# Kernel tuning notes

Hardware: AMD Instinct MI355X
Metric: run time of the kernel (lower is better)

## Reference

```python
import jax, jax.numpy as jnp
import numpy as np

B, S, D = 1, 2048, 4096
HQ, HK, HD = 32, 8, 128


def setup_inputs() -> dict:
    key = jax.random.key(0)
    ks = jax.random.split(key, 6)
    x = jax.random.normal(ks[0], (B, S, D), jnp.float32) * 0.02
    wq = jax.random.normal(ks[1], (D, HQ * HD), jnp.float32) * 0.02
    wk = jax.random.normal(ks[2], (D, HK * HD), jnp.float32) * 0.02
    wv = jax.random.normal(ks[3], (D, HK * HD), jnp.float32) * 0.02
    wo = jax.random.normal(ks[4], (HQ * HD, D), jnp.float32) * 0.02
    # canonical RoPE frequencies: theta = 10000
    inv_freq = 1.0 / (10000.0 ** (jnp.arange(0, HD, 2, dtype=jnp.float32) / HD))  # [HD/2]
    t = jnp.arange(S, dtype=jnp.float32)
    ang = jnp.outer(t, inv_freq)  # [S, HD/2]
    return {
        "x": x,
        "freqs_cos": jnp.cos(ang),
        "freqs_sin": jnp.sin(ang),
        "wq": wq, "wk": wk, "wv": wv, "wo": wo,
    }


def _rope(t, cos, sin):
    # t: [B, S, H, HD]; pairs are consecutive elements (view_as_complex semantics)
    tr = t.reshape(*t.shape[:-1], HD // 2, 2)
    t0, t1 = tr[..., 0], tr[..., 1]
    c = cos[None, :, None, :]
    s = sin[None, :, None, :]
    o0 = t0 * c - t1 * s
    o1 = t0 * s + t1 * c
    return jnp.stack([o0, o1], axis=-1).reshape(t.shape)


def reference(x, freqs_cos, freqs_sin, wq, wk, wv, wo):
    b, s, _ = x.shape
    g = HQ // HK  # GQA group size
    xq = (x @ wq).reshape(b, s, HQ, HD)
    xk = (x @ wk).reshape(b, s, HK, HD)
    xv = (x @ wv).reshape(b, s, HK, HD)
    xq = _rope(xq, freqs_cos, freqs_sin)
    xk = _rope(xk, freqs_cos, freqs_sin)
    scale = 1.0 / jnp.sqrt(jnp.float32(HD))
    xqg = xq.reshape(b, s, HK, g, HD)
    # scores: [b, HK, g, s_q, s_k]
    scores = jnp.einsum("bqkgd,bnkd->bkgqn", xqg, xk) * scale
    causal = jnp.tril(jnp.ones((s, s), dtype=bool))
    scores = jnp.where(causal[None, None, None, :, :], scores, -jnp.inf)
    p = jax.nn.softmax(scores, axis=-1)
    out = jnp.einsum("bkgqn,bnkd->bqkgd", p, xv).reshape(b, s, HQ * HD)
    return out @ wo
```

## Files before the change

kernel.cpp:

```cpp
#include <hip/hip_runtime.h>
#include <stdint.h>

typedef __bf16 bf16_t;
typedef bf16_t bf16x8 __attribute__((ext_vector_type(8)));
typedef float f32x4 __attribute__((ext_vector_type(4)));
typedef unsigned int u32;
typedef unsigned short u16;

#define DEV_INLINE __device__ __forceinline__

#define S_LEN 2048
#define D_MODEL 4096
#define HQ 32
#define HK 8
#define HD 128
#define NQKV 6144

DEV_INLINE u16 f2bf(float x) {
  union { float f; uint32_t u; } v; v.f = x;
  uint32_t r = v.u + 0x7FFFu + ((v.u >> 16) & 1u);
  return (u16)(r >> 16);
}
DEV_INLINE float bf2f(u16 x) {
  union { uint32_t u; float f; } v; v.u = ((uint32_t)x) << 16;
  return v.f;
}
DEV_INLINE u32 pack2bf(float a, float b) {
  return (u32)f2bf(a) | ((u32)f2bf(b) << 16);
}

DEV_INLINE void async_load16(const void* g, void* l) {
  __builtin_amdgcn_global_load_lds(
      (const __attribute__((address_space(1))) u32*)g,
      (__attribute__((address_space(3))) u32*)l, 16, 0, 0);
}

DEV_INLINE f32x4 mfma16(bf16x8 a, bf16x8 b, f32x4 c) {
  return __builtin_amdgcn_mfma_f32_16x16x32_bf16(a, b, c, 0, 0, 0);
}

__global__ void cvt_f32_bf16(const float* __restrict__ in, u16* __restrict__ out, int n) {
  int i = (blockIdx.x * blockDim.x + threadIdx.x) * 4;
  if (i >= n) return;
  float4 v = *(const float4*)(in + i);
  union { u16 s[4]; uint2 u; } o;
  o.s[0] = f2bf(v.x); o.s[1] = f2bf(v.y); o.s[2] = f2bf(v.z); o.s[3] = f2bf(v.w);
  *(uint2*)(out + i) = o.u;
}

__global__ void transpose_f32_bf16(const float* __restrict__ in, u16* __restrict__ out,
                                   int R, int C) {
  __shared__ float tile[32][33];
  int tx = threadIdx.x, ty = threadIdx.y;
  int c0 = blockIdx.x * 32, r0 = blockIdx.y * 32;
#pragma unroll
  for (int i = 0; i < 4; ++i)
    tile[ty + i * 8][tx] = in[(long)(r0 + ty + i * 8) * C + c0 + tx];
  __syncthreads();
#pragma unroll
  for (int i = 0; i < 4; ++i)
    out[(long)(c0 + ty + i * 8) * R + r0 + tx] = f2bf(tile[tx][ty + i * 8]);
}

__global__ void transpose_bf16(const u16* __restrict__ in, u16* __restrict__ out,
                               int R, int C, int ld_in, int col_off) {
  __shared__ u16 tile[32][33];
  int tx = threadIdx.x, ty = threadIdx.y;
  int c0 = blockIdx.x * 32, r0 = blockIdx.y * 32;
#pragma unroll
  for (int i = 0; i < 4; ++i)
    tile[ty + i * 8][tx] = in[(long)(r0 + ty + i * 8) * ld_in + col_off + c0 + tx];
  __syncthreads();
#pragma unroll
  for (int i = 0; i < 4; ++i)
    out[(long)(c0 + ty + i * 8) * R + r0 + tx] = tile[tx][ty + i * 8];
}

__global__ void rope_bf16(const u16* __restrict__ in, const float* __restrict__ cosb,
                          const float* __restrict__ sinb, u16* __restrict__ out,
                          int H, int ld_in, int col_off, float scale) {
  int idx = blockIdx.x * blockDim.x + threadIdx.x;
  int j = idx & 63;
  int sh = idx >> 6;
  int s = sh / H, h = sh - s * H;
  const u16* ip = in + (long)s * ld_in + col_off + h * HD;
  union { u32 u; u16 s2[2]; } v; v.u = *(const u32*)(ip + 2 * j);
  float q0 = bf2f(v.s2[0]), q1 = bf2f(v.s2[1]);
  float c = cosb[s * 64 + j], sn = sinb[s * 64 + j];
  union { u16 s2[2]; u32 u; } o;
  o.s2[0] = f2bf((q0 * c - q1 * sn) * scale);
  o.s2[1] = f2bf((q0 * sn + q1 * c) * scale);
  *(u32*)(out + (long)sh * HD + 2 * j) = o.u;
}

#define BARRIER() asm volatile("s_barrier" ::: "memory")
#define WAIT_LGKM0()                                            \
  do {                                                          \
    asm volatile("s_waitcnt lgkmcnt(0)" ::: "memory");          \
    __builtin_amdgcn_sched_barrier(0);                          \
  } while (0)
#define WAIT_VM(N) asm volatile("s_waitcnt vmcnt(" #N ")" ::: "memory")

#define PHASE_A(T, DO_STAGE)                                                      \
  {                                                                               \
    const u16* Ab_ = &lds[(T) & 3][0];                                            \
    const u16* Bb_ = &lds[(T) & 3][8192];                                         \
    bf16x8 af_[MFH];                                                              \
    _Pragma("unroll")                                                             \
    for (int i = 0; i < MFH; ++i) af_[i] = rdfrag(Ab_, wr * MROWS + i * 16 + l15);\
    _Pragma("unroll")                                                             \
    for (int j = 0; j < 4; ++j) bfr[j] = rdfrag(Bb_, wc * 64 + j * 16 + l15);     \
    if (DO_STAGE) stageA((T) + 3);                                                \
    BARRIER();                                                                    \
    WAIT_LGKM0();                                                                 \
    __builtin_amdgcn_s_setprio(1);                                                \
    _Pragma("unroll")                                                             \
    for (int i = 0; i < MFH; ++i)                                                 \
      _Pragma("unroll")                                                           \
      for (int j = 0; j < 4; ++j) acc[i][j] = mfma16(af_[i], bfr[j], acc[i][j]);  \
    __builtin_amdgcn_s_setprio(0);                                                \
    BARRIER();                                                                    \
  }

#define PHASE_B(T, DO_STAGE, VMWAIT)                                              \
  {                                                                               \
    const u16* Ab_ = &lds[(T) & 3][0];                                            \
    bf16x8 af_[MFH];                                                              \
    _Pragma("unroll")                                                             \
    for (int i = 0; i < MFH; ++i)                                                 \
      af_[i] = rdfrag(Ab_, wr * MROWS + (MFH + i) * 16 + l15);                    \
    if (DO_STAGE) stageB((T) + 3);                                                \
    BARRIER();                                                                    \
    WAIT_LGKM0();                                                                 \
    __builtin_amdgcn_s_setprio(1);                                                \
    _Pragma("unroll")                                                             \
    for (int i = 0; i < MFH; ++i)                                                 \
      _Pragma("unroll")                                                           \
      for (int j = 0; j < 4; ++j)                                                 \
        acc[MFH + i][j] = mfma16(af_[i], bfr[j], acc[MFH + i][j]);                \
    __builtin_amdgcn_s_setprio(0);                                                \
    VMWAIT;                                                                       \
    BARRIER();                                                                    \
  }

template <int BN, int WM, bool BF16OUT>
__global__ __launch_bounds__(512, 2) void gemm_pipe(
    const u16* __restrict__ A, const u16* __restrict__ Bt, void* __restrict__ Cv,
    int N, int K) {
  constexpr int WN = 8 / WM;
  constexpr int MROWS = 256 / WM;
  constexpr int MF = MROWS / 16;
  constexpr int MFH = MF / 2;
  constexpr int BPT = (BN * 4) / 512;
  constexpr int LDSU = (256 + BN) * 32;

  __shared__ __attribute__((aligned(16))) u16 lds[4][LDSU];

  const int tid = threadIdx.x;
  const int lane = tid & 63;
  const int wave = tid >> 6;
  const int quad = lane >> 4, l15 = lane & 15;
  const int wr = wave / WN, wc = wave % WN;

  const int gx = gridDim.x;
  const int bid = blockIdx.y * gx + blockIdx.x;
  const int cpx = (gx * gridDim.y) >> 3;
  const int sw = (bid & 7) * cpx + (bid >> 3);
  const int bn = sw % gx, bm = sw / gx;

  const long arow = (long)bm * 256, brow = (long)bn * BN;
  const int NT = K >> 5;

  auto stageA = [&](int ts) {
    const int bs = ts & 3;
    const int k0 = ts * 32;
#pragma unroll
    for (int j = 0; j < 2; ++j) {
      int c = tid + j * 512;
      int row = c >> 2, cc = c & 3, cs = cc ^ ((row >> 1) & 3);
      async_load16(A + (arow + row) * (long)K + k0 + cs * 8,
                   (u16*)&lds[bs][0] + c * 8);
    }
  };
  auto stageB = [&](int ts) {
    const int bs = ts & 3;
    const int k0 = ts * 32;
#pragma unroll
    for (int j = 0; j < BPT; ++j) {
      int c = tid + j * 512;
      int row = c >> 2, cc = c & 3, cs = cc ^ ((row >> 1) & 3);
      async_load16(Bt + (brow + row) * (long)K + k0 + cs * 8,
                   (u16*)&lds[bs][8192] + c * 8);
    }
  };
  auto rdfrag = [&](const u16* base, int row) -> bf16x8 {
    return *(const bf16x8*)(base + row * 32 + ((quad ^ ((row >> 1) & 3)) * 8));
  };

  f32x4 acc[MF][4] = {};
  bf16x8 bfr[4];

  stageA(0); stageB(0); stageA(1); stageB(1); stageA(2); stageB(2);
  if constexpr (BN == 256) { WAIT_VM(8); } else { WAIT_VM(6); }
  BARRIER();

  int t = 0;
  for (; t < NT - 3; ++t) {
    PHASE_A(t, true);
    if constexpr (BN == 256) { PHASE_B(t, true, WAIT_VM(8)); }
    else                     { PHASE_B(t, true, WAIT_VM(6)); }
  }
  PHASE_A(t, false);
  if constexpr (BN == 256) { PHASE_B(t, false, WAIT_VM(4)); }
  else                     { PHASE_B(t, false, WAIT_VM(3)); }
  ++t;
  PHASE_A(t, false);
  PHASE_B(t, false, WAIT_VM(0));
  ++t;
  PHASE_A(t, false);
  PHASE_B(t, false, ((void)0));

#pragma unroll
  for (int i = 0; i < MF; ++i) {
    const long row = (long)bm * 256 + wr * MROWS + i * 16 + quad * 4;
#pragma unroll
    for (int j = 0; j < 4; ++j) {
      const int col = bn * BN + wc * 64 + j * 16 + l15;
      if constexpr (BF16OUT) {
        u16* C = (u16*)Cv;
#pragma unroll
        for (int r = 0; r < 4; ++r) C[(row + r) * N + col] = f2bf(acc[i][j][r]);
      } else {
        float* C = (float*)Cv;
#pragma unroll
        for (int r = 0; r < 4; ++r) C[(row + r) * N + col] = acc[i][j][r];
      }
    }
  }
}

#define NEG_INF -1e30f
__global__ __launch_bounds__(256, 2) void attn_fwd(
    const u16* __restrict__ Qb, const u16* __restrict__ Kb,
    const u16* __restrict__ Vt, u16* __restrict__ Ob) {
  __shared__ __attribute__((aligned(16))) u16 Ks[2][64 * 128];
  __shared__ __attribute__((aligned(16))) u16 Vs[2][128 * 64];
  __shared__ __attribute__((aligned(16))) u16 Pts[4][16 * 64];
  const int tid = threadIdx.x;
  const int lane = tid & 63, wave = tid >> 6;
  const int quad = lane >> 4, l15 = lane & 15;
  const int lin = blockIdx.y * gridDim.x + blockIdx.x;
  const int h = lin & 31;
  const int pp = (lin >> 5) & 7;
  const int u = (lin >> 8) ? 15 - pp : pp;
  const int hk = h >> 2;
  const int swz = 2 * (l15 & 7);
  const int nt = 2 * (u + 1);

  bf16x8 qf[2][4];
#pragma unroll
  for (int n = 0; n < 2; ++n) {
    const u16* qrow = Qb + (long)(u * 128 + wave * 32 + n * 16 + l15) * (HQ * HD)
                      + h * HD + quad * 8;
#pragma unroll
    for (int ks = 0; ks < 4; ++ks) qf[n][ks] = *(const bf16x8*)(qrow + ks * 32);
  }

  auto stage = [&](int t) {
    const int b = t & 1;
#pragma unroll
    for (int it = 0; it < 4; ++it) {
      int c = tid + it * 256;
      int row = c >> 4, cc = c & 15, cs = cc ^ (row & 15);
      async_load16(Kb + (long)(t * 64 + row) * (HK * HD) + hk * HD + cs * 8,
                   (u16*)&Ks[b][0] + c * 8);
    }
#pragma unroll
    for (int it = 0; it < 4; ++it) {
      int c = tid + it * 256;
      int row = c >> 3, cc = c & 7, cs = cc ^ (row & 7);
      async_load16(Vt + (long)(hk * HD + row) * S_LEN + t * 64 + cs * 8,
                   (u16*)&Vs[b][0] + c * 8);
    }
  };

  float m_run[2] = {NEG_INF, NEG_INF}, l_run[2] = {0.f, 0.f};
  f32x4 oacc[8][2] = {};

  stage(0);
  __syncthreads();

  for (int t = 0; t < nt; ++t) {
    const int cur = t & 1;
    if (t + 1 < nt) stage(t + 1);

    if (t * 64 <= u * 128 + wave * 32 + 31) {
      f32x4 sc[4][2] = {};
      __builtin_amdgcn_s_setprio(1);
#pragma unroll
      for (int ks = 0; ks < 4; ++ks)
#pragma unroll
        for (int tj = 0; tj < 4; ++tj) {
          int row = tj * 16 + l15;
          bf16x8 kf = *(const bf16x8*)(&Ks[cur][0] + row * 128
                                       + (((ks * 4 + quad) ^ (row & 15)) * 8));
          sc[tj][0] = mfma16(kf, qf[0][ks], sc[tj][0]);
          sc[tj][1] = mfma16(kf, qf[1][ks], sc[tj][1]);
        }
      __builtin_amdgcn_s_setprio(0);

      const bool diag = (t >= 2 * u);
      const int kbase = t * 64 - u * 128;
#pragma unroll
      for (int n = 0; n < 2; ++n) {
        int qloc = wave * 32 + n * 16 + l15;
        if (diag) {
#pragma unroll
          for (int tj = 0; tj < 4; ++tj)
#pragma unroll
            for (int r = 0; r < 4; ++r)
              if (kbase + tj * 16 + quad * 4 + r > qloc) sc[tj][n][r] = NEG_INF;
        }
        float m = NEG_INF;
#pragma unroll
        for (int tj = 0; tj < 4; ++tj)
#pragma unroll
          for (int r = 0; r < 4; ++r) m = fmaxf(m, sc[tj][n][r]);
        m = fmaxf(m, __shfl_xor(m, 16));
        m = fmaxf(m, __shfl_xor(m, 32));
        if (!__all(m - m_run[n] <= 8.0f)) {
          float mnew = fmaxf(m_run[n], m);
          float alpha = __expf(m_run[n] - mnew);
          m_run[n] = mnew;
          l_run[n] *= alpha;
#pragma unroll
          for (int tj = 0; tj < 8; ++tj) oacc[tj][n] *= alpha;
        }
        float rs = 0.f;
#pragma unroll
        for (int tj = 0; tj < 4; ++tj)
#pragma unroll
          for (int r = 0; r < 4; ++r) {
            float p = __expf(sc[tj][n][r] - m_run[n]);
            sc[tj][n][r] = p;
            rs += p;
          }
        rs += __shfl_xor(rs, 16);
        rs += __shfl_xor(rs, 32);
        l_run[n] += rs;
      }

      u16* pw = &Pts[wave][0];
      bf16x8 pf0[2], pf1[2];
#pragma unroll
      for (int tj = 0; tj < 4; ++tj) {
        union { u32 w[2]; uint2 u2; } pk;
        pk.w[0] = pack2bf(sc[tj][0][0], sc[tj][0][1]);
        pk.w[1] = pack2bf(sc[tj][0][2], sc[tj][0][3]);
        *(uint2*)(pw + l15 * 64 + (((tj * 4 + quad) ^ swz) * 4)) = pk.u2;
      }
      __asm__ volatile("s_waitcnt lgkmcnt(0)" ::: "memory");
#pragma unroll
      for (int ks = 0; ks < 2; ++ks)
        pf0[ks] = *(const bf16x8*)(pw + l15 * 64 + (((ks * 8 + quad * 2) ^ swz) * 4));
      __asm__ volatile("s_waitcnt lgkmcnt(0)" ::: "memory");
#pragma unroll
      for (int tj = 0; tj < 4; ++tj) {
        union { u32 w[2]; uint2 u2; } pk;
        pk.w[0] = pack2bf(sc[tj][1][0], sc[tj][1][1]);
        pk.w[1] = pack2bf(sc[tj][1][2], sc[tj][1][3]);
        *(uint2*)(pw + l15 * 64 + (((tj * 4 + quad) ^ swz) * 4)) = pk.u2;
      }
      __asm__ volatile("s_waitcnt lgkmcnt(0)" ::: "memory");
#pragma unroll
      for (int ks = 0; ks < 2; ++ks)
        pf1[ks] = *(const bf16x8*)(pw + l15 * 64 + (((ks * 8 + quad * 2) ^ swz) * 4));

      __builtin_amdgcn_s_setprio(1);
#pragma unroll
      for (int ks = 0; ks < 2; ++ks)
#pragma unroll
        for (int tj = 0; tj < 8; ++tj) {
          int row = tj * 16 + l15;
          bf16x8 vf = *(const bf16x8*)(&Vs[cur][0] + row * 64
                                       + (((ks * 4 + quad) ^ (row & 7)) * 8));
          oacc[tj][0] = mfma16(vf, pf0[ks], oacc[tj][0]);
          oacc[tj][1] = mfma16(vf, pf1[ks], oacc[tj][1]);
        }
      __builtin_amdgcn_s_setprio(0);
    }

    __syncthreads();
  }

#pragma unroll
  for (int n = 0; n < 2; ++n) {
    float inv_l = 1.0f / l_run[n];
    long grow = u * 128 + wave * 32 + n * 16 + l15;
#pragma unroll
    for (int tj = 0; tj < 8; ++tj) {
      int gcol = h * HD + tj * 16 + quad * 4;
      union { u32 w[2]; uint2 u2; } pk;
      pk.w[0] = pack2bf(oacc[tj][n][0] * inv_l, oacc[tj][n][1] * inv_l);
      pk.w[1] = pack2bf(oacc[tj][n][2] * inv_l, oacc[tj][n][3] * inv_l);
      *(uint2*)(Ob + grow * (HQ * HD) + gcol) = pk.u2;
    }
  }
}

#define MB (1024L * 1024L)

extern "C" void kernel_launch(void* const* d_in, const int* in_sizes, int n_in,
                              void* d_out, int out_size, void* d_ws, size_t ws_size,
                              hipStream_t stream) {
  const float* x    = (const float*)d_in[0];
  const float* fcos = (const float*)d_in[1];
  const float* fsin = (const float*)d_in[2];
  const float* wq   = (const float*)d_in[3];
  const float* wk   = (const float*)d_in[4];
  const float* wv   = (const float*)d_in[5];
  const float* wo   = (const float*)d_in[6];
  float* out = (float*)d_out;

  char* ws = (char*)d_ws;
  u16* wt    = (u16*)(ws + 0 * MB);
  u16* xb    = (u16*)(ws + 48 * MB);
  u16* QKVb  = (u16*)(ws + 64 * MB);
  u16* Qb    = (u16*)(ws + 88 * MB);
  u16* Kb    = (u16*)(ws + 104 * MB);
  u16* Vt    = (u16*)(ws + 108 * MB);
  u16* attnb = (u16*)(ws + 112 * MB);

  const int M = S_LEN, D = D_MODEL;

  cvt_f32_bf16<<<(M * D) / 1024, 256, 0, stream>>>(x, xb, M * D);

  transpose_f32_bf16<<<dim3(D / 32, D / 32), dim3(32, 8), 0, stream>>>(wq, wt, D, HQ * HD);
  transpose_f32_bf16<<<dim3((HK * HD) / 32, D / 32), dim3(32, 8), 0, stream>>>(
      wk, wt + (long)(HQ * HD) * D, D, HK * HD);
  transpose_f32_bf16<<<dim3((HK * HD) / 32, D / 32), dim3(32, 8), 0, stream>>>(
      wv, wt + (long)(HQ * HD + HK * HD) * D, D, HK * HD);

  gemm_pipe<256, 2, true><<<dim3(NQKV / 256, M / 256), 512, 0, stream>>>(
      xb, wt, QKVb, NQKV, D);

  rope_bf16<<<(M * HQ * 64) / 256, 256, 0, stream>>>(
      QKVb, fcos, fsin, Qb, HQ, NQKV, 0, 0.08838834764831845f);
  rope_bf16<<<(M * HK * 64) / 256, 256, 0, stream>>>(
      QKVb, fcos, fsin, Kb, HK, NQKV, HQ * HD, 1.0f);
  transpose_bf16<<<dim3((HK * HD) / 32, M / 32), dim3(32, 8), 0, stream>>>(
      QKVb, Vt, M, HK * HD, NQKV, HQ * HD + HK * HD);

  attn_fwd<<<dim3(16, HQ), 256, 0, stream>>>(Qb, Kb, Vt, attnb);

  transpose_f32_bf16<<<dim3(D / 32, D / 32), dim3(32, 8), 0, stream>>>(wo, wt, HQ * HD, D);
  gemm_pipe<128, 4, false><<<dim3(D / 128, M / 256), 512, 0, stream>>>(
      attnb, wt, out, D, HQ * HD);
}
```

Measured before the change: 493.5 us.

## Generalize GEMM tile width and use 192-wide tiles for QKV projection

Parameterizes the pipelined GEMM over per-wave column fragments so non-power-of-two tile widths work, and switches the QKV projection to 256x192 tiles. The grid grows from 24x8 to 32x8 blocks, which is meant to fill the CUs more evenly. It also drops the explicit lgkmcnt(0) wait and sched_barrier before the MFMA blocks, leaving LDS-read waits to the compiler. The B-stage load for 192 columns has some threads duplicate loads (c-256), which adds redundant traffic, and removing the explicit wait could affect correctness or scheduling.

```diff
diff --git a/kernel.cpp b/kernel.cpp
--- a/kernel.cpp
+++ b/kernel.cpp
@@ -94,11 +94,6 @@
 }
 
 #define BARRIER() asm volatile("s_barrier" ::: "memory")
-#define WAIT_LGKM0()                                            \
-  do {                                                          \
-    asm volatile("s_waitcnt lgkmcnt(0)" ::: "memory");          \
-    __builtin_amdgcn_sched_barrier(0);                          \
-  } while (0)
 #define WAIT_VM(N) asm volatile("s_waitcnt vmcnt(" #N ")" ::: "memory")
 
 #define PHASE_A(T, DO_STAGE)                                                      \
@@ -109,15 +104,14 @@
     _Pragma("unroll")                                                             \
     for (int i = 0; i < MFH; ++i) af_[i] = rdfrag(Ab_, wr * MROWS + i * 16 + l15);\
     _Pragma("unroll")                                                             \
-    for (int j = 0; j < 4; ++j) bfr[j] = rdfrag(Bb_, wc * 64 + j * 16 + l15);     \
+    for (int j = 0; j < NF; ++j) bfr[j] = rdfrag(Bb_, wc * WCOLS + j * 16 + l15); \
     if (DO_STAGE) stageA((T) + 3);                                                \
     BARRIER();                                                                    \
-    WAIT_LGKM0();                                                                 \
     __builtin_amdgcn_s_setprio(1);                                                \
     _Pragma("unroll")                                                             \
     for (int i = 0; i < MFH; ++i)                                                 \
       _Pragma("unroll")                                                           \
-      for (int j = 0; j < 4; ++j) acc[i][j] = mfma16(af_[i], bfr[j], acc[i][j]);  \
+      for (int j = 0; j < NF; ++j) acc[i][j] = mfma16(af_[i], bfr[j], acc[i][j]); \
     __builtin_amdgcn_s_setprio(0);                                                \
     BARRIER();                                                                    \
   }
@@ -131,12 +125,11 @@
       af_[i] = rdfrag(Ab_, wr * MROWS + (MFH + i) * 16 + l15);                    \
     if (DO_STAGE) stageB((T) + 3);                                                \
     BARRIER();                                                                    \
-    WAIT_LGKM0();                                                                 \
     __builtin_amdgcn_s_setprio(1);                                                \
     _Pragma("unroll")                                                             \
     for (int i = 0; i < MFH; ++i)                                                 \
       _Pragma("unroll")                                                           \
-      for (int j = 0; j < 4; ++j)                                                 \
+      for (int j = 0; j < NF; ++j)                                                \
         acc[MFH + i][j] = mfma16(af_[i], bfr[j], acc[MFH + i][j]);                \
     __builtin_amdgcn_s_setprio(0);                                                \
     VMWAIT;                                                                       \
@@ -151,7 +144,10 @@
   constexpr int MROWS = 256 / WM;
   constexpr int MF = MROWS / 16;
   constexpr int MFH = MF / 2;
-  constexpr int BPT = (BN * 4) / 512;
+  constexpr int NF = BN / (WN * 16);
+  constexpr int WCOLS = NF * 16;
+  constexpr int BCH = BN * 4;
+  constexpr int BISS = (BCH + 511) / 512;
   constexpr int LDSU = (256 + BN) * 32;
 
   __shared__ __attribute__((aligned(16))) u16 lds[4][LDSU];
@@ -186,32 +182,33 @@
     const int bs = ts & 3;
     const int k0 = ts * 32;
 #pragma unroll
-    for (int j = 0; j < BPT; ++j) {
+    for (int j = 0; j < BISS; ++j) {
       int c = tid + j * 512;
-      int row = c >> 2, cc = c & 3, cs = cc ^ ((row >> 1) & 3);
+      int cd = (c < BCH) ? c : c - 256;
+      int row = cd >> 2, cc = cd & 3, cs = cc ^ ((row >> 1) & 3);
       async_load16(Bt + (brow + row) * (long)K + k0 + cs * 8,
-                   (u16*)&lds[bs][8192] + c * 8);
+                   (u16*)&lds[bs][8192] + cd * 8);
     }
   };
   auto rdfrag = [&](const u16* base, int row) -> bf16x8 {
     return *(const bf16x8*)(base + row * 32 + ((quad ^ ((row >> 1) & 3)) * 8));
   };
 
-  f32x4 acc[MF][4] = {};
-  bf16x8 bfr[4];
+  f32x4 acc[MF][NF] = {};
+  bf16x8 bfr[NF];
 
   stageA(0); stageB(0); stageA(1); stageB(1); stageA(2); stageB(2);
-  if constexpr (BN == 256) { WAIT_VM(8); } else { WAIT_VM(6); }
+  if constexpr (BISS == 2) { WAIT_VM(8); } else { WAIT_VM(6); }
   BARRIER();
 
   int t = 0;
   for (; t < NT - 3; ++t) {
     PHASE_A(t, true);
-    if constexpr (BN == 256) { PHASE_B(t, true, WAIT_VM(8)); }
+    if constexpr (BISS == 2) { PHASE_B(t, true, WAIT_VM(8)); }
     else                     { PHASE_B(t, true, WAIT_VM(6)); }
   }
   PHASE_A(t, false);
-  if constexpr (BN == 256) { PHASE_B(t, false, WAIT_VM(4)); }
+  if constexpr (BISS == 2) { PHASE_B(t, false, WAIT_VM(4)); }
   else                     { PHASE_B(t, false, WAIT_VM(3)); }
   ++t;
   PHASE_A(t, false);
@@ -224,8 +221,8 @@
   for (int i = 0; i < MF; ++i) {
     const long row = (long)bm * 256 + wr * MROWS + i * 16 + quad * 4;
 #pragma unroll
-    for (int j = 0; j < 4; ++j) {
-      const int col = bn * BN + wc * 64 + j * 16 + l15;
+    for (int j = 0; j < NF; ++j) {
+      const int col = bn * BN + wc * WCOLS + j * 16 + l15;
       if constexpr (BF16OUT) {
         u16* C = (u16*)Cv;
 #pragma unroll
@@ -441,7 +438,7 @@
   transpose_f32_bf16<<<dim3((HK * HD) / 32, D / 32), dim3(32, 8), 0, stream>>>(
       wv, wt + (long)(HQ * HD + HK * HD) * D, D, HK * HD);
 
-  gemm_pipe<256, 2, true><<<dim3(NQKV / 256, M / 256), 512, 0, stream>>>(
+  gemm_pipe<192, 2, true><<<dim3(NQKV / 192, M / 256), 512, 0, stream>>>(
       xb, wt, QKVb, NQKV, D);
 
   rope_bf16<<<(M * HQ * 64) / 256, 256, 0, stream>>>(
```

After: 487.8 us. Within noise of the previous version (-1.2%).
